# Kernel optimization log

Hardware: AMD Instinct MI355X
Metric: run time of the kernel (lower is better)

The kernel has to match this reference:

```python
import jax, jax.numpy as jnp
import numpy as np

SEQ_LEN, INPUT_DIM, HIDDEN_DIM, NUM_CLASSES, BATCH = 512, 256, 1024, 128, 256


def setup_inputs() -> dict:
    key = jax.random.key(0)
    ks = jax.random.split(key, 12)
    sx = np.sqrt(2.0 / INPUT_DIM).astype(np.float32)
    sh = np.sqrt(2.0 / HIDDEN_DIM).astype(np.float32)
    inp = {
        "x": jax.random.randint(ks[0], (BATCH, SEQ_LEN, 1), 0, NUM_CLASSES, dtype=jnp.int32),
        "emb": jax.random.normal(ks[1], (NUM_CLASSES, INPUT_DIM), jnp.float32),
        "Wcx": jax.random.normal(ks[2], (HIDDEN_DIM, INPUT_DIM), jnp.float32) * sx,
        "bc": jnp.zeros((HIDDEN_DIM,), jnp.float32),
        "Wix": jax.random.normal(ks[3], (HIDDEN_DIM, INPUT_DIM), jnp.float32) * sx,
        "Wih": jax.random.normal(ks[4], (HIDDEN_DIM, HIDDEN_DIM), jnp.float32) * sh,
        "bi": jnp.zeros((HIDDEN_DIM,), jnp.float32),
        "Wfx": jax.random.normal(ks[5], (HIDDEN_DIM, INPUT_DIM), jnp.float32) * sx,
        "Wfh": jax.random.normal(ks[6], (HIDDEN_DIM, HIDDEN_DIM), jnp.float32) * sh,
        "bf": jnp.zeros((HIDDEN_DIM,), jnp.float32),
        "Wox": jax.random.normal(ks[7], (HIDDEN_DIM, INPUT_DIM), jnp.float32) * sx,
        "Woh": jax.random.normal(ks[8], (HIDDEN_DIM, HIDDEN_DIM), jnp.float32) * sh,
        "bo": jnp.zeros((HIDDEN_DIM,), jnp.float32),
        "Wph": jax.random.normal(ks[9], (NUM_CLASSES, HIDDEN_DIM), jnp.float32) * sh,
        "bp": jnp.zeros((NUM_CLASSES,), jnp.float32),
    }
    return inp


def reference(x, emb, Wcx, bc, Wix, Wih, bi, Wfx, Wfh, bf, Wox, Woh, bo, Wph, bp):
    B = x.shape[0]
    H = Wfh.shape[0]
    xt = emb[x[:, :, 0]]                       # [B, S, I] embedded inputs
    # Precompute the input-to-gate projections (parallel over time; identical math)
    xf = jnp.einsum("bsi,hi->sbh", xt, Wfx)    # [S, B, H]
    xi = jnp.einsum("bsi,hi->sbh", xt, Wix)
    xo = jnp.einsum("bsi,hi->sbh", xt, Wox)
    xc = jnp.einsum("bsi,hi->sbh", xt, Wcx)

    def step(carry, inputs):
        c, h = carry
        xf_t, xi_t, xo_t, xc_t = inputs
        # peephole gates read cell state c, not h
        f = jax.nn.sigmoid(xf_t + c @ Wfh.T + bf)
        i = jax.nn.sigmoid(xi_t + c @ Wih.T + bi)
        o = jax.nn.sigmoid(xo_t + c @ Woh.T + bo)
        c_new = jax.nn.sigmoid(xc_t + bc) * i + c * f
        h_new = jnp.tanh(c_new) * o
        return (c_new, h_new), None

    c0 = jnp.zeros((B, H), xt.dtype)
    h0 = jnp.zeros((B, H), xt.dtype)
    (c_T, h_T), _ = jax.lax.scan(step, (c0, h0), (xf, xi, xo, xc))
    p = h_T @ Wph.T + bp                       # [B, num_classes]
    return jax.nn.log_softmax(p, axis=1)
```

## Files before the change

### kernel.cpp

```cpp
#include <hip/hip_runtime.h>

#define SEQ  512
#define IDIM 256
#define H    1024
#define NC   128
#define B    256
#define NBLK 256

typedef __attribute__((ext_vector_type(8))) short bh8;
typedef __attribute__((ext_vector_type(4))) float f4;
typedef __attribute__((ext_vector_type(4))) int i4;

__device__ __forceinline__ float sigf(float x) { return 1.0f / (1.0f + __expf(-x)); }

__device__ __forceinline__ unsigned short bf16r(float v) {
    unsigned u = __builtin_bit_cast(unsigned, v);
    u += 0x7fffu + ((u >> 16) & 1u);
    return (unsigned short)(u >> 16);
}

__global__ __launch_bounds__(256) void tables_kernel(
    const float* __restrict__ emb,
    const float* __restrict__ Wcx, const float* __restrict__ bc,
    const float* __restrict__ Wix, const float* __restrict__ bi,
    const float* __restrict__ Wfx, const float* __restrict__ bf,
    const float* __restrict__ Wox, const float* __restrict__ bo,
    float* __restrict__ FF, float* __restrict__ II,
    float* __restrict__ OO, float* __restrict__ G)
{
    const int k = blockIdx.x;
    const int h = blockIdx.y * 256 + threadIdx.x;
    __shared__ float e[IDIM];
    e[threadIdx.x] = emb[k * IDIM + threadIdx.x];
    __syncthreads();
    const float4* e4  = (const float4*)e;
    const float4* wf4 = (const float4*)(Wfx + (size_t)h * IDIM);
    const float4* wi4 = (const float4*)(Wix + (size_t)h * IDIM);
    const float4* wo4 = (const float4*)(Wox + (size_t)h * IDIM);
    const float4* wc4 = (const float4*)(Wcx + (size_t)h * IDIM);
    float aF = 0.f, aI = 0.f, aO = 0.f, aC = 0.f;
#pragma unroll 4
    for (int i = 0; i < IDIM / 4; i++) {
        float4 ev = e4[i];
        float4 a = wf4[i]; aF += ev.x * a.x + ev.y * a.y + ev.z * a.z + ev.w * a.w;
        float4 b = wi4[i]; aI += ev.x * b.x + ev.y * b.y + ev.z * b.z + ev.w * b.w;
        float4 c = wo4[i]; aO += ev.x * c.x + ev.y * c.y + ev.z * c.z + ev.w * c.w;
        float4 d = wc4[i]; aC += ev.x * d.x + ev.y * d.y + ev.z * d.z + ev.w * d.w;
    }
    const int o = k * H + h;
    FF[o] = aF + bf[h];
    II[o] = aI + bi[h];
    OO[o] = aO + bo[h];
    G[o]  = sigf(aC + bc[h]);
}

__global__ __launch_bounds__(256) void swz_kernel(const float* __restrict__ W,
                                                  unsigned short* __restrict__ D)
{
    int g = blockIdx.x * 256 + threadIdx.x;
    int h  = g >> 7;
    int kc = (g & 127) << 3;
    const float4* s = (const float4*)(W + (size_t)h * H + kc);
    float4 a = s[0], b = s[1];
    unsigned short tmp[8] = { bf16r(a.x), bf16r(a.y), bf16r(a.z), bf16r(a.w),
                              bf16r(b.x), bf16r(b.y), bf16r(b.z), bf16r(b.w) };
    int nb = h >> 4, kb = kc >> 5, quad = (kc >> 3) & 3;
    int lane = (h & 15) + (quad << 4);
    bh8 v;
#pragma unroll
    for (int j = 0; j < 8; j++) v[j] = (short)tmp[j];
    *(bh8*)(D + (size_t)((nb * 32 + kb) * 512 + lane * 8)) = v;
}

__global__ __launch_bounds__(256, 1) void persist_kernel(
    const unsigned short* __restrict__ Wf, const unsigned short* __restrict__ Wi,
    const unsigned short* __restrict__ Wo,
    const float* __restrict__ FF, const float* __restrict__ II,
    const float* __restrict__ OO, const float* __restrict__ G,
    const int* __restrict__ x,
    unsigned short* c16a, unsigned short* c16b,
    float* __restrict__ hb, int* flags)
{
    const int blk = blockIdx.x;
    const int rt = blk >> 4;
    const int nt = blk & 15;
    const int tid  = threadIdx.x;
    const int wave = tid >> 6;
    const int lane = tid & 63;
    const int l15 = lane & 15, quad = lane >> 4;

    __shared__ unsigned short cs[16 * 1024];

    const int row0 = rt * 16;
    const int abase = l15 * 1024;
    const int asw = l15 & 7;
    const int hcol = nt * 64 + wave * 16 + l15;
    const int nb = nt * 4 + wave;

    const unsigned short* wfp = Wf + (size_t)nb * 32 * 512 + (size_t)lane * 8;
    const unsigned short* wip = Wi + (size_t)nb * 32 * 512 + (size_t)lane * 8;
    const unsigned short* wop = Wo + (size_t)nb * 32 * 512 + (size_t)lane * 8;

    bh8 wf_r[32], wi_r[32];
#pragma unroll
    for (int kt = 0; kt < 32; kt++) {
        wf_r[kt] = *(const bh8*)(wfp + (size_t)kt * 512);
        wi_r[kt] = *(const bh8*)(wip + (size_t)kt * 512);
    }

    float cn_keep[4] = {0.f, 0.f, 0.f, 0.f};
    int* const myflag = flags + rt * 64 + nt * 4 + wave;
    const int* const pf = flags + rt * 64 + lane;

    for (int s = 0; s < SEQ; s++) {
        const unsigned short* cur16 = (s & 1) ? c16b : c16a;
        unsigned short*       nxt16 = (s & 1) ? c16a : c16b;

        float ffv[4], iiv[4], ggv[4];
#pragma unroll
        for (int r = 0; r < 4; r++) {
            int b = row0 + quad * 4 + r;
            int tok = x[b * SEQ + s];
            ffv[r] = FF[tok * H + hcol];
            iiv[r] = II[tok * H + hcol];
            ggv[r] = G[tok * H + hcol];
        }

        f4 accF = {0.f, 0.f, 0.f, 0.f}, accI = {0.f, 0.f, 0.f, 0.f};
        if (s > 0) {
            {
                int guard = 0;
                for (;;) {
                    int fv;
                    asm volatile("global_load_dword %0, %1, off sc0 sc1\n\ts_waitcnt vmcnt(0)"
                                 : "=v"(fv) : "v"(pf) : "memory");
                    if (__all(fv >= s)) break;
                    if (++guard > (1 << 20)) break;
                }
            }
            i4 tmp[8];
#pragma unroll
            for (int i = 0; i < 8; i++) {
                int chunk = i * 256 + tid;
                int row = chunk >> 7, g = chunk & 127;
                const i4* p = (const i4*)(cur16 + (size_t)(row0 + row) * H + g * 8);
                asm volatile("global_load_dwordx4 %0, %1, off sc0 sc1"
                             : "=v"(tmp[i]) : "v"(p));
            }
            asm volatile("s_waitcnt vmcnt(0)" ::: "memory");
#pragma unroll
            for (int i = 0; i < 8; i++) {
                int chunk = i * 256 + tid;
                int row = chunk >> 7, g = chunk & 127;
                *(i4*)(cs + row * 1024 + ((g ^ (row & 7)) << 3)) = tmp[i];
            }
            __syncthreads();
#pragma unroll
            for (int kt = 0; kt < 32; kt++) {
                bh8 a = *(const bh8*)(cs + abase + (((kt * 4 + quad) ^ asw) << 3));
                accF = __builtin_amdgcn_mfma_f32_16x16x32_bf16(a, wf_r[kt], accF, 0, 0, 0);
                accI = __builtin_amdgcn_mfma_f32_16x16x32_bf16(a, wi_r[kt], accI, 0, 0, 0);
            }
        }

#pragma unroll
        for (int r = 0; r < 4; r++) {
            float f = sigf(ffv[r] + accF[r]);
            float i = sigf(iiv[r] + accI[r]);
            float cn = ggv[r] * i + cn_keep[r] * f;
            cn_keep[r] = cn;
            int b = row0 + quad * 4 + r;
            unsigned us = bf16r(cn);
            unsigned ot = (unsigned)__shfl_xor((int)us, 1);
            if (s < SEQ - 1 && (lane & 1) == 0)
                __hip_atomic_store((unsigned*)(nxt16 + (size_t)b * H + hcol), us | (ot << 16),
                                   __ATOMIC_RELAXED, __HIP_MEMORY_SCOPE_AGENT);
        }

        if (s < SEQ - 1) {
            asm volatile("s_waitcnt vmcnt(0)" ::: "memory");
            if (lane == 0) {
                int v = s + 1;
                asm volatile("global_store_dword %0, %1, off sc0 sc1"
                             :: "v"(myflag), "v"(v) : "memory");
            }
        }
    }

    f4 accO = {0.f, 0.f, 0.f, 0.f};
#pragma unroll 4
    for (int kt = 0; kt < 32; kt++) {
        bh8 a  = *(const bh8*)(cs + abase + (((kt * 4 + quad) ^ asw) << 3));
        bh8 bo = *(const bh8*)(wop + (size_t)kt * 512);
        accO = __builtin_amdgcn_mfma_f32_16x16x32_bf16(a, bo, accO, 0, 0, 0);
    }
#pragma unroll
    for (int r = 0; r < 4; r++) {
        int b = row0 + quad * 4 + r;
        int tok = x[b * SEQ + (SEQ - 1)];
        float o = sigf(OO[tok * H + hcol] + accO[r]);
        hb[(size_t)b * H + hcol] = tanhf(cn_keep[r]) * o;
    }
}

__global__ __launch_bounds__(128) void out_kernel(
    const float* __restrict__ hbuf, const float* __restrict__ Wph,
    const float* __restrict__ bp, float* __restrict__ out)
{
    const int b = blockIdx.x;
    const int j = threadIdx.x;
    __shared__ float hs[H];
    for (int t = j; t < H; t += 128) hs[t] = hbuf[(size_t)b * H + t];
    __syncthreads();
    const float4* w4 = (const float4*)(Wph + (size_t)j * H);
    const float4* h4 = (const float4*)hs;
    float acc = bp[j];
#pragma unroll 4
    for (int k = 0; k < H / 4; k++) {
        float4 a = w4[k], v = h4[k];
        acc += a.x * v.x + a.y * v.y + a.z * v.z + a.w * v.w;
    }
    __shared__ float red[128];
    red[j] = acc; __syncthreads();
    for (int off = 64; off > 0; off >>= 1) { if (j < off) red[j] = fmaxf(red[j], red[j + off]); __syncthreads(); }
    float m = red[0]; __syncthreads();
    red[j] = __expf(acc - m); __syncthreads();
    for (int off = 64; off > 0; off >>= 1) { if (j < off) red[j] += red[j + off]; __syncthreads(); }
    float lse = m + __logf(red[0]);
    out[(size_t)b * NC + j] = acc - lse;
}

extern "C" void kernel_launch(void* const* d_in, const int* in_sizes, int n_in,
                              void* d_out, int out_size, void* d_ws, size_t ws_size,
                              hipStream_t stream)
{
    const int*   x   = (const int*)d_in[0];
    const float* emb = (const float*)d_in[1];
    const float* Wcx = (const float*)d_in[2];
    const float* bc  = (const float*)d_in[3];
    const float* Wix = (const float*)d_in[4];
    const float* Wih = (const float*)d_in[5];
    const float* bi  = (const float*)d_in[6];
    const float* Wfx = (const float*)d_in[7];
    const float* Wfh = (const float*)d_in[8];
    const float* bf  = (const float*)d_in[9];
    const float* Wox = (const float*)d_in[10];
    const float* Woh = (const float*)d_in[11];
    const float* bo  = (const float*)d_in[12];
    const float* Wph = (const float*)d_in[13];
    const float* bp  = (const float*)d_in[14];
    float* out = (float*)d_out;

    char* wsb = (char*)d_ws;
    float* FF = (float*)(wsb + 0);
    float* II = (float*)(wsb + (512 << 10));
    float* OO = (float*)(wsb + (1024 << 10));
    float* G  = (float*)(wsb + (1536 << 10));
    float* hb = (float*)(wsb + (2048 << 10));
    int*   flags = (int*)(wsb + (3072 << 10));
    unsigned short* Wf_sw = (unsigned short*)(wsb + (4096 << 10));
    unsigned short* Wi_sw = (unsigned short*)(wsb + (6144 << 10));
    unsigned short* Wo_sw = (unsigned short*)(wsb + (8192 << 10));
    unsigned short* c16a  = (unsigned short*)(wsb + (10240 << 10));
    unsigned short* c16b  = (unsigned short*)(wsb + (10752 << 10));

    hipMemsetAsync(flags, 0, 4096, stream);

    tables_kernel<<<dim3(NC, 4), 256, 0, stream>>>(emb, Wcx, bc, Wix, bi, Wfx, bf, Wox, bo,
                                                   FF, II, OO, G);
    swz_kernel<<<512, 256, 0, stream>>>(Wfh, Wf_sw);
    swz_kernel<<<512, 256, 0, stream>>>(Wih, Wi_sw);
    swz_kernel<<<512, 256, 0, stream>>>(Woh, Wo_sw);

    persist_kernel<<<NBLK, 256, 0, stream>>>(Wf_sw, Wi_sw, Wo_sw, FF, II, OO, G, x,
                                             c16a, c16b, hb, flags);

    out_kernel<<<B, 128, 0, stream>>>(hb, Wph, bp, out);
}
```

Baseline: 2.320 ms.

## Load recurrent cell-state fragments directly from global with pipelined register buffers

Drops the shared-memory staging of the bf16 cell state and the per-step __syncthreads. Each wave now loads its own MFMA A fragments straight from global/L2 into two register buffers of eight vectors, with partial s_waitcnt so the loads overlap the MFMAs. The final output-gate matmul is rewritten the same way, reading c16b. The goal is to remove the LDS round trip and the block barrier from the serial recurrence, at the cost of four-fold redundant L2 reads across waves and higher register pressure.

```diff
diff --git a/kernel.cpp b/kernel.cpp
--- a/kernel.cpp
+++ b/kernel.cpp
@@ -9,7 +9,6 @@
 
 typedef __attribute__((ext_vector_type(8))) short bh8;
 typedef __attribute__((ext_vector_type(4))) float f4;
-typedef __attribute__((ext_vector_type(4))) int i4;
 
 __device__ __forceinline__ float sigf(float x) { return 1.0f / (1.0f + __expf(-x)); }
 
@@ -89,11 +88,7 @@
     const int lane = tid & 63;
     const int l15 = lane & 15, quad = lane >> 4;
 
-    __shared__ unsigned short cs[16 * 1024];
-
     const int row0 = rt * 16;
-    const int abase = l15 * 1024;
-    const int asw = l15 & 7;
     const int hcol = nt * 64 + wave * 16 + l15;
     const int nb = nt * 4 + wave;
 
@@ -111,6 +106,8 @@
     float cn_keep[4] = {0.f, 0.f, 0.f, 0.f};
     int* const myflag = flags + rt * 64 + nt * 4 + wave;
     const int* const pf = flags + rt * 64 + lane;
+
+    const size_t aoff = (size_t)(row0 + l15) * H + quad * 8;
 
     for (int s = 0; s < SEQ; s++) {
         const unsigned short* cur16 = (s & 1) ? c16b : c16a;
@@ -138,28 +135,39 @@
                     if (++guard > (1 << 20)) break;
                 }
             }
-            i4 tmp[8];
-#pragma unroll
-            for (int i = 0; i < 8; i++) {
-                int chunk = i * 256 + tid;
-                int row = chunk >> 7, g = chunk & 127;
-                const i4* p = (const i4*)(cur16 + (size_t)(row0 + row) * H + g * 8);
+            const unsigned short* arow = cur16 + aoff;
+            bh8 a0[8], a1[8];
+#pragma unroll
+            for (int j = 0; j < 8; j++)
                 asm volatile("global_load_dwordx4 %0, %1, off sc0 sc1"
-                             : "=v"(tmp[i]) : "v"(p));
-            }
-            asm volatile("s_waitcnt vmcnt(0)" ::: "memory");
-#pragma unroll
-            for (int i = 0; i < 8; i++) {
-                int chunk = i * 256 + tid;
-                int row = chunk >> 7, g = chunk & 127;
-                *(i4*)(cs + row * 1024 + ((g ^ (row & 7)) << 3)) = tmp[i];
-            }
-            __syncthreads();
-#pragma unroll
-            for (int kt = 0; kt < 32; kt++) {
-                bh8 a = *(const bh8*)(cs + abase + (((kt * 4 + quad) ^ asw) << 3));
-                accF = __builtin_amdgcn_mfma_f32_16x16x32_bf16(a, wf_r[kt], accF, 0, 0, 0);
-                accI = __builtin_amdgcn_mfma_f32_16x16x32_bf16(a, wi_r[kt], accI, 0, 0, 0);
+                             : "=v"(a0[j]) : "v"(arow + j * 32));
+#pragma unroll
+            for (int j = 0; j < 8; j++)
+                asm volatile("global_load_dwordx4 %0, %1, off sc0 sc1"
+                             : "=v"(a1[j]) : "v"(arow + (8 + j) * 32));
+#pragma unroll
+            for (int b = 0; b < 4; b++) {
+                bh8* cur = (b & 1) ? a1 : a0;
+                if (b < 3)
+                    asm volatile("s_waitcnt vmcnt(8)"
+                        : "+v"(cur[0]), "+v"(cur[1]), "+v"(cur[2]), "+v"(cur[3]),
+                          "+v"(cur[4]), "+v"(cur[5]), "+v"(cur[6]), "+v"(cur[7]) :: "memory");
+                else
+                    asm volatile("s_waitcnt vmcnt(0)"
+                        : "+v"(cur[0]), "+v"(cur[1]), "+v"(cur[2]), "+v"(cur[3]),
+                          "+v"(cur[4]), "+v"(cur[5]), "+v"(cur[6]), "+v"(cur[7]) :: "memory");
+#pragma unroll
+                for (int j = 0; j < 8; j++) {
+                    int kt = b * 8 + j;
+                    accF = __builtin_amdgcn_mfma_f32_16x16x32_bf16(cur[j], wf_r[kt], accF, 0, 0, 0);
+                    accI = __builtin_amdgcn_mfma_f32_16x16x32_bf16(cur[j], wi_r[kt], accI, 0, 0, 0);
+                }
+                if (b < 2) {
+#pragma unroll
+                    for (int j = 0; j < 8; j++)
+                        asm volatile("global_load_dwordx4 %0, %1, off sc0 sc1"
+                                     : "=v"(cur[j]) : "v"(arow + ((b + 2) * 8 + j) * 32));
+                }
             }
         }
 
@@ -187,19 +195,49 @@
         }
     }
 
-    f4 accO = {0.f, 0.f, 0.f, 0.f};
-#pragma unroll 4
-    for (int kt = 0; kt < 32; kt++) {
-        bh8 a  = *(const bh8*)(cs + abase + (((kt * 4 + quad) ^ asw) << 3));
-        bh8 bo = *(const bh8*)(wop + (size_t)kt * 512);
-        accO = __builtin_amdgcn_mfma_f32_16x16x32_bf16(a, bo, accO, 0, 0, 0);
-    }
-#pragma unroll
-    for (int r = 0; r < 4; r++) {
-        int b = row0 + quad * 4 + r;
-        int tok = x[b * SEQ + (SEQ - 1)];
-        float o = sigf(OO[tok * H + hcol] + accO[r]);
-        hb[(size_t)b * H + hcol] = tanhf(cn_keep[r]) * o;
+    {
+        const unsigned short* arow = c16b + aoff;
+        f4 accO = {0.f, 0.f, 0.f, 0.f};
+        bh8 a0[8], a1[8];
+#pragma unroll
+        for (int j = 0; j < 8; j++)
+            asm volatile("global_load_dwordx4 %0, %1, off sc0 sc1"
+                         : "=v"(a0[j]) : "v"(arow + j * 32));
+#pragma unroll
+        for (int j = 0; j < 8; j++)
+            asm volatile("global_load_dwordx4 %0, %1, off sc0 sc1"
+                         : "=v"(a1[j]) : "v"(arow + (8 + j) * 32));
+#pragma unroll
+        for (int b = 0; b < 4; b++) {
+            bh8* cur = (b & 1) ? a1 : a0;
+            if (b < 3)
+                asm volatile("s_waitcnt vmcnt(8)"
+                    : "+v"(cur[0]), "+v"(cur[1]), "+v"(cur[2]), "+v"(cur[3]),
+                      "+v"(cur[4]), "+v"(cur[5]), "+v"(cur[6]), "+v"(cur[7]) :: "memory");
+            else
+                asm volatile("s_waitcnt vmcnt(0)"
+                    : "+v"(cur[0]), "+v"(cur[1]), "+v"(cur[2]), "+v"(cur[3]),
+                      "+v"(cur[4]), "+v"(cur[5]), "+v"(cur[6]), "+v"(cur[7]) :: "memory");
+#pragma unroll
+            for (int j = 0; j < 8; j++) {
+                int kt = b * 8 + j;
+                bh8 bo = *(const bh8*)(wop + (size_t)kt * 512);
+                accO = __builtin_amdgcn_mfma_f32_16x16x32_bf16(cur[j], bo, accO, 0, 0, 0);
+            }
+            if (b < 2) {
+#pragma unroll
+                for (int j = 0; j < 8; j++)
+                    asm volatile("global_load_dwordx4 %0, %1, off sc0 sc1"
+                                 : "=v"(cur[j]) : "v"(arow + ((b + 2) * 8 + j) * 32));
+            }
+        }
+#pragma unroll
+        for (int r = 0; r < 4; r++) {
+            int b = row0 + quad * 4 + r;
+            int tok = x[b * SEQ + (SEQ - 1)];
+            float o = sigf(OO[tok * H + hcol] + accO[r]);
+            hb[(size_t)b * H + hcol] = tanhf(cn_keep[r]) * o;
+        }
     }
 }
 
```

After: 3.499 ms. 50.8% more time.
